# Optimization experiments

Hardware: AMD Instinct MI355X
Metric: run time of the kernel (lower is better)

## Reference

```python
import jax, jax.numpy as jnp
import numpy as np
from jax import lax

LBDA = 0.5   # soft-min temperature from OTAM_cum_dist_v2 default
EPS = 0.01   # cos_sim epsilon


def otam_cum_dist(dists, lbda=LBDA):
    """Soft-DTW-style OTAM DP. dists: [nq, ns, L, S] -> [nq, ns].
    Faithful to OTAM_cum_dist_v2: pad last dim by (1,1) with zeros, then run the
    row-wise recurrence. Soft-min computed via stable logsumexp (same math as
    -lbda*log(sum exp(-x/lbda)))."""
    nq, ns, L, S = dists.shape
    d = jnp.pad(dists, ((0, 0), (0, 0), (0, 0), (1, 1)))  # [nq, ns, L, W], W=S+2
    W = S + 2
    # Row 0: cum[0, m] = cum[0, m-1] + d[0, m], cum[0, 0] = 0
    row0 = jnp.concatenate(
        [jnp.zeros((nq, ns, 1), d.dtype), jnp.cumsum(d[:, :, 0, 1:], axis=-1)], axis=-1)
    if L == 1:
        return row0[..., -1]

    m_idx = jnp.arange(1, W)
    include_up = (m_idx == 1) | (m_idx == W - 1)  # only first/last cols use cum[l-1, m]
    INF = jnp.asarray(jnp.inf, d.dtype)

    def row_step(prev_row, d_row):
        # prev_row, d_row: [nq, ns, W]
        xs = (
            jnp.moveaxis(d_row[:, :, 1:], -1, 0),        # d[l, m],       [W-1, nq, ns]
            jnp.moveaxis(prev_row[:, :, :-1], -1, 0),    # cum[l-1, m-1]
            jnp.moveaxis(prev_row[:, :, 1:], -1, 0),     # cum[l-1, m]
            include_up,
        )

        def col_step(cur_left, x):
            d_m, p_diag, p_up, inc = x
            up = jnp.where(inc, p_up, INF)               # masked term -> exp(-inf)=0
            terms = jnp.stack([p_diag, cur_left, up])    # [3, nq, ns]
            new = d_m - lbda * jax.nn.logsumexp(-terms / lbda, axis=0)
            return new, new

        _, cols = lax.scan(col_step, jnp.zeros((nq, ns), d.dtype), xs)
        row = jnp.concatenate(
            [jnp.zeros((nq, ns, 1), d.dtype), jnp.moveaxis(cols, 0, -1)], axis=-1)
        return row, None

    d_rows = jnp.moveaxis(d[:, :, 1:, :], 2, 0)          # [L-1, nq, ns, W]
    final_row, _ = lax.scan(row_step, row0, d_rows)
    return final_row[..., -1]


def reference(support_features, query_features):
    """OTAM meta-logits (cum_dist_g = -otam_distance) of DSN_TEMPORAL.
    support_features: [n_classes, L, D] class prototypes; query_features: [nq, L, D]."""
    nq, Lq, D = query_features.shape
    ns, Ls, _ = support_features.shape
    q = query_features.reshape(nq * Lq, D)
    s = support_features.reshape(ns * Ls, D)
    # cos_sim with epsilon in denominator (faithful to cos_sim())
    num = q @ s.T
    den = (jnp.linalg.norm(q, axis=-1)[:, None]
           * jnp.linalg.norm(s, axis=-1)[None, :] + EPS)
    frame_dists = 1.0 - num / den                         # [nq*L, ns*S]
    dists = frame_dists.reshape(nq, Lq, ns, Ls).transpose(0, 2, 1, 3)  # [nq, ns, L, S]
    cum = otam_cum_dist(dists) + otam_cum_dist(dists.transpose(0, 1, 3, 2))
    return -cum                                           # meta_logits [nq, ns]


def setup_inputs() -> dict:
    key = jax.random.key(0)
    k1, k2 = jax.random.split(key)
    return {
        "support_features": jax.random.normal(k1, (64, 8, 576), dtype=jnp.float32),
        "query_features": jax.random.normal(k2, (2048, 8, 576), dtype=jnp.float32),
    }
```

## Files before the change

### kernel.cpp

```cpp
#include <hip/hip_runtime.h>

#define D_K 576
#define NSLAB 18
#define LBDA_INV 2.0f
#define HALF_LBDA 0.5f
#define EPS 0.01f
#define DSTRIDE 136
#define DT_STRIDE 72
#define POOL_USHORTS 17920

typedef __attribute__((ext_vector_type(8))) short short8;
typedef __attribute__((ext_vector_type(4))) float f32x4;

__device__ inline unsigned cvt_pk_bf16(float lo, float hi) {
    unsigned r;
    asm("v_cvt_pk_bf16_f32 %0, %1, %2" : "=v"(r) : "v"(lo), "v"(hi));
    return r;
}

__device__ inline float softmin2(float a, float b) {
    float mn = fminf(a, b), mx = fmaxf(a, b);
    return mn - HALF_LBDA * __logf(1.f + __expf(LBDA_INV * (mn - mx)));
}
__device__ inline float softmin3(float a, float b, float c) {
    float mn = fminf(fminf(a, b), c);
    float mx = fmaxf(fmaxf(a, b), c);
    float md = __builtin_amdgcn_fmed3f(a, b, c);
    float s = 1.f + __expf(LBDA_INV * (mn - md)) + __expf(LBDA_INV * (mn - mx));
    return mn - HALF_LBDA * __logf(s);
}

template <int STRIDE>
__device__ float otam_dp_rows(const unsigned short* base) {
    float x[8], prev[10], cur[10];
    auto load_row = [&](int l) {
        uint4 v = *(const uint4*)(base + l * STRIDE);
        x[0] = __uint_as_float(v.x << 16);
        x[1] = __uint_as_float(v.x & 0xFFFF0000u);
        x[2] = __uint_as_float(v.y << 16);
        x[3] = __uint_as_float(v.y & 0xFFFF0000u);
        x[4] = __uint_as_float(v.z << 16);
        x[5] = __uint_as_float(v.z & 0xFFFF0000u);
        x[6] = __uint_as_float(v.w << 16);
        x[7] = __uint_as_float(v.w & 0xFFFF0000u);
    };
    load_row(0);
    prev[0] = 0.f;
#pragma unroll
    for (int m = 1; m <= 8; ++m) prev[m] = prev[m - 1] + x[m - 1];
    prev[9] = prev[8];
#pragma unroll
    for (int l = 1; l < 8; ++l) {
        load_row(l);
        cur[0] = 0.f;
        cur[1] = x[0] + softmin3(prev[0], 0.f, prev[1]);
#pragma unroll
        for (int m = 2; m <= 8; ++m)
            cur[m] = x[m - 1] + softmin2(prev[m - 1], cur[m - 1]);
        cur[9] = softmin3(prev[8], cur[8], prev[9]);
#pragma unroll
        for (int m = 0; m < 10; ++m) prev[m] = cur[m];
    }
    return prev[9];
}

__global__ __launch_bounds__(256, 4) void fused_kernel(
        const float* __restrict__ sup, const float* __restrict__ qry,
        float* __restrict__ out) {
    __shared__ __align__(16) unsigned short pool[POOL_USHORTS];
    __shared__ float qn_l[64], sn_l[128];
    unsigned short* const As0 = pool;
    unsigned short* const Bs0 = pool + 2048;
    unsigned short* const As1 = pool + 6144;
    unsigned short* const Bs1 = pool + 8192;
    unsigned short* const Ds  = pool;
    unsigned short* const DsT = pool + 8704;

    const int t = threadIdx.x;
    const int b = blockIdx.x;
    const int xcd = b & 7, s2 = b >> 3;
    const int sblk = s2 >> 5;
    const int qh = xcd * 32 + (s2 & 31);

    const float* qsrc = qry + (size_t)qh * 64 * D_K;
    const float* ssrc = sup + (size_t)sblk * 128 * D_K;

    const int rr = t >> 3;
    const int cc = t & 7;
    const int c_in = cc >> 1, half = cc & 1;

    const int lane = t & 63;
    const int wave = t >> 6;
    const int wm = wave >> 1, wn = wave & 1;
    const int col16 = lane & 15, quad = lane >> 4;

    f32x4 acc[2][4];
#pragma unroll
    for (int i = 0; i < 2; ++i)
#pragma unroll
        for (int j = 0; j < 4; ++j) acc[i][j] = (f32x4){0.f, 0.f, 0.f, 0.f};

    int aoff[2], boff[4], woffA[2], woffB[4];
#pragma unroll
    for (int mt = 0; mt < 2; ++mt) {
        int m = wm * 32 + mt * 16 + col16;
        aoff[mt] = (quad * 64 + (m ^ (quad << 1))) * 8;
    }
#pragma unroll
    for (int nt = 0; nt < 4; ++nt) {
        int n = wn * 64 + nt * 16 + col16;
        boff[nt] = (quad * 128 + (n ^ (quad << 1))) * 8;
    }
#pragma unroll
    for (int j = 0; j < 2; ++j)
        woffA[j] = (c_in * 64 + ((j * 32 + rr) ^ (c_in << 1))) * 8 + half * 4;
#pragma unroll
    for (int j = 0; j < 4; ++j)
        woffB[j] = (c_in * 128 + ((j * 32 + rr) ^ (c_in << 1))) * 8 + half * 4;

    float ssA[2] = {0.f, 0.f}, ssB[4] = {0.f, 0.f, 0.f, 0.f};
    float4 va[2], vb[4];

    auto stage_load = [&](int sl) {
        const int off = sl * 32 + cc * 4;
#pragma unroll
        for (int j = 0; j < 2; ++j)
            va[j] = *(const float4*)(qsrc + (size_t)(j * 32 + rr) * D_K + off);
#pragma unroll
        for (int j = 0; j < 4; ++j)
            vb[j] = *(const float4*)(ssrc + (size_t)(j * 32 + rr) * D_K + off);
    };
    auto stage_write = [&](unsigned short* __restrict__ A,
                           unsigned short* __restrict__ B) {
#pragma unroll
        for (int j = 0; j < 2; ++j) {
            ssA[j] += va[j].x * va[j].x + va[j].y * va[j].y +
                      va[j].z * va[j].z + va[j].w * va[j].w;
            uint2 u;
            u.x = cvt_pk_bf16(va[j].x, va[j].y);
            u.y = cvt_pk_bf16(va[j].z, va[j].w);
            *(uint2*)(&A[woffA[j]]) = u;
        }
#pragma unroll
        for (int j = 0; j < 4; ++j) {
            ssB[j] += vb[j].x * vb[j].x + vb[j].y * vb[j].y +
                      vb[j].z * vb[j].z + vb[j].w * vb[j].w;
            uint2 u;
            u.x = cvt_pk_bf16(vb[j].x, vb[j].y);
            u.y = cvt_pk_bf16(vb[j].z, vb[j].w);
            *(uint2*)(&B[woffB[j]]) = u;
        }
    };
    auto compute = [&](const unsigned short* __restrict__ A,
                       const unsigned short* __restrict__ B) {
        short8 af[2], bq[4];
#pragma unroll
        for (int mt = 0; mt < 2; ++mt) af[mt] = *(const short8*)(&A[aoff[mt]]);
#pragma unroll
        for (int nt = 0; nt < 4; ++nt) bq[nt] = *(const short8*)(&B[boff[nt]]);
#pragma unroll
        for (int mt = 0; mt < 2; ++mt)
#pragma unroll
            for (int nt = 0; nt < 4; ++nt)
                acc[mt][nt] = __builtin_amdgcn_mfma_f32_16x16x32_bf16(
                    af[mt], bq[nt], acc[mt][nt], 0, 0, 0);
    };

    stage_load(0);
    stage_write(As0, Bs0);
    __syncthreads();

#pragma unroll 1
    for (int sp = 0; sp < 9; ++sp) {
        stage_load(2 * sp + 1);
        compute(As0, Bs0);
        stage_write(As1, Bs1);
        __syncthreads();
        if (sp < 8) stage_load(2 * sp + 2);
        compute(As1, Bs1);
        if (sp < 8) stage_write(As0, Bs0);
        __syncthreads();
    }

#pragma unroll
    for (int j = 0; j < 2; ++j) {
        float a = ssA[j];
        a += __shfl_down(a, 4); a += __shfl_down(a, 2); a += __shfl_down(a, 1);
        if ((t & 7) == 0) qn_l[j * 32 + rr] = sqrtf(a);
    }
#pragma unroll
    for (int j = 0; j < 4; ++j) {
        float s = ssB[j];
        s += __shfl_down(s, 4); s += __shfl_down(s, 2); s += __shfl_down(s, 1);
        if ((t & 7) == 0) sn_l[j * 32 + rr] = sqrtf(s);
    }
    __syncthreads();

#pragma unroll
    for (int mt = 0; mt < 2; ++mt) {
        const int m = wm * 32 + mt * 16 + quad * 4;
        float q0 = qn_l[m], q1 = qn_l[m + 1], q2 = qn_l[m + 2], q3 = qn_l[m + 3];
#pragma unroll
        for (int nt = 0; nt < 4; ++nt) {
            const int n = wn * 64 + nt * 16 + col16;
            float sv = sn_l[n];
            float d0 = 1.f - acc[mt][nt][0] * __builtin_amdgcn_rcpf(q0 * sv + EPS);
            float d1 = 1.f - acc[mt][nt][1] * __builtin_amdgcn_rcpf(q1 * sv + EPS);
            float d2 = 1.f - acc[mt][nt][2] * __builtin_amdgcn_rcpf(q2 * sv + EPS);
            float d3 = 1.f - acc[mt][nt][3] * __builtin_amdgcn_rcpf(q3 * sv + EPS);
            uint2 u;
            u.x = cvt_pk_bf16(d0, d1);
            u.y = cvt_pk_bf16(d2, d3);
            *(uint2*)(&DsT[n * DT_STRIDE + m]) = u;
            Ds[(m + 0) * DSTRIDE + n] = (unsigned short)(u.x);
            Ds[(m + 1) * DSTRIDE + n] = (unsigned short)(u.x >> 16);
            Ds[(m + 2) * DSTRIDE + n] = (unsigned short)(u.y);
            Ds[(m + 3) * DSTRIDE + n] = (unsigned short)(u.y >> 16);
        }
    }
    __syncthreads();

    const int p = t & 127, ql = p >> 4, sj = p & 15;
    float r;
    if (t < 128) {
        r = otam_dp_rows<DSTRIDE>(Ds + (ql * 8) * DSTRIDE + sj * 8);
    } else {
        r = otam_dp_rows<DT_STRIDE>(DsT + (sj * 8) * DT_STRIDE + ql * 8);
        sn_l[p] = r;
    }
    __syncthreads();
    if (t < 128) {
        int qg = qh * 8 + ql, sg = sblk * 16 + sj;
        out[qg * 64 + sg] = -(r + sn_l[p]);
    }
}

extern "C" void kernel_launch(void* const* d_in, const int* in_sizes, int n_in,
                              void* d_out, int out_size, void* d_ws, size_t ws_size,
                              hipStream_t stream) {
    const float* sup = (const float*)d_in[0];
    const float* qry = (const float*)d_in[1];
    float* out = (float*)d_out;
    (void)d_ws; (void)ws_size;
    fused_kernel<<<dim3(1024), dim3(256), 0, stream>>>(sup, qry, out);
}
```

Before: 105.6 us.

## Load query operand directly from global into MFMA registers, bypassing LDS

```diff
diff --git a/kernel.cpp b/kernel.cpp
--- a/kernel.cpp
+++ b/kernel.cpp
@@ -69,10 +69,8 @@
         float* __restrict__ out) {
     __shared__ __align__(16) unsigned short pool[POOL_USHORTS];
     __shared__ float qn_l[64], sn_l[128];
-    unsigned short* const As0 = pool;
-    unsigned short* const Bs0 = pool + 2048;
-    unsigned short* const As1 = pool + 6144;
-    unsigned short* const Bs1 = pool + 8192;
+    unsigned short* const Bs0 = pool;
+    unsigned short* const Bs1 = pool + 4096;
     unsigned short* const Ds  = pool;
     unsigned short* const DsT = pool + 8704;
 
@@ -100,47 +98,31 @@
 #pragma unroll
         for (int j = 0; j < 4; ++j) acc[i][j] = (f32x4){0.f, 0.f, 0.f, 0.f};
 
-    int aoff[2], boff[4], woffA[2], woffB[4];
-#pragma unroll
-    for (int mt = 0; mt < 2; ++mt) {
-        int m = wm * 32 + mt * 16 + col16;
-        aoff[mt] = (quad * 64 + (m ^ (quad << 1))) * 8;
-    }
+    int agoff[2];
+#pragma unroll
+    for (int mt = 0; mt < 2; ++mt)
+        agoff[mt] = (wm * 32 + mt * 16 + col16) * D_K + quad * 8;
+
+    int boff[4], woff[4];
 #pragma unroll
     for (int nt = 0; nt < 4; ++nt) {
         int n = wn * 64 + nt * 16 + col16;
         boff[nt] = (quad * 128 + (n ^ (quad << 1))) * 8;
     }
 #pragma unroll
-    for (int j = 0; j < 2; ++j)
-        woffA[j] = (c_in * 64 + ((j * 32 + rr) ^ (c_in << 1))) * 8 + half * 4;
-#pragma unroll
     for (int j = 0; j < 4; ++j)
-        woffB[j] = (c_in * 128 + ((j * 32 + rr) ^ (c_in << 1))) * 8 + half * 4;
+        woff[j] = (c_in * 128 + ((j * 32 + rr) ^ (c_in << 1))) * 8 + half * 4;
 
     float ssA[2] = {0.f, 0.f}, ssB[4] = {0.f, 0.f, 0.f, 0.f};
-    float4 va[2], vb[4];
+    float4 vb[4];
 
     auto stage_load = [&](int sl) {
         const int off = sl * 32 + cc * 4;
 #pragma unroll
-        for (int j = 0; j < 2; ++j)
-            va[j] = *(const float4*)(qsrc + (size_t)(j * 32 + rr) * D_K + off);
-#pragma unroll
         for (int j = 0; j < 4; ++j)
             vb[j] = *(const float4*)(ssrc + (size_t)(j * 32 + rr) * D_K + off);
     };
-    auto stage_write = [&](unsigned short* __restrict__ A,
-                           unsigned short* __restrict__ B) {
-#pragma unroll
-        for (int j = 0; j < 2; ++j) {
-            ssA[j] += va[j].x * va[j].x + va[j].y * va[j].y +
-                      va[j].z * va[j].z + va[j].w * va[j].w;
-            uint2 u;
-            u.x = cvt_pk_bf16(va[j].x, va[j].y);
-            u.y = cvt_pk_bf16(va[j].z, va[j].w);
-            *(uint2*)(&A[woffA[j]]) = u;
-        }
+    auto stage_write = [&](unsigned short* __restrict__ B) {
 #pragma unroll
         for (int j = 0; j < 4; ++j) {
             ssB[j] += vb[j].x * vb[j].x + vb[j].y * vb[j].y +
@@ -148,16 +130,34 @@
             uint2 u;
             u.x = cvt_pk_bf16(vb[j].x, vb[j].y);
             u.y = cvt_pk_bf16(vb[j].z, vb[j].w);
-            *(uint2*)(&B[woffB[j]]) = u;
-        }
-    };
-    auto compute = [&](const unsigned short* __restrict__ A,
-                       const unsigned short* __restrict__ B) {
-        short8 af[2], bq[4];
-#pragma unroll
-        for (int mt = 0; mt < 2; ++mt) af[mt] = *(const short8*)(&A[aoff[mt]]);
+            *(uint2*)(&B[woff[j]]) = u;
+        }
+    };
+    auto compute = [&](int sl, const unsigned short* __restrict__ B) {
+        float4 a0[2], a1[2];
+#pragma unroll
+        for (int mt = 0; mt < 2; ++mt) {
+            const float* ap = qsrc + agoff[mt] + sl * 32;
+            a0[mt] = *(const float4*)(ap);
+            a1[mt] = *(const float4*)(ap + 4);
+        }
+        short8 bq[4];
 #pragma unroll
         for (int nt = 0; nt < 4; ++nt) bq[nt] = *(const short8*)(&B[boff[nt]]);
+        short8 af[2];
+#pragma unroll
+        for (int mt = 0; mt < 2; ++mt) {
+            ssA[mt] += a0[mt].x * a0[mt].x + a0[mt].y * a0[mt].y +
+                       a0[mt].z * a0[mt].z + a0[mt].w * a0[mt].w +
+                       a1[mt].x * a1[mt].x + a1[mt].y * a1[mt].y +
+                       a1[mt].z * a1[mt].z + a1[mt].w * a1[mt].w;
+            uint4 u;
+            u.x = cvt_pk_bf16(a0[mt].x, a0[mt].y);
+            u.y = cvt_pk_bf16(a0[mt].z, a0[mt].w);
+            u.z = cvt_pk_bf16(a1[mt].x, a1[mt].y);
+            u.w = cvt_pk_bf16(a1[mt].z, a1[mt].w);
+            af[mt] = *(short8*)&u;
+        }
 #pragma unroll
         for (int mt = 0; mt < 2; ++mt)
 #pragma unroll
@@ -167,26 +167,27 @@
     };
 
     stage_load(0);
-    stage_write(As0, Bs0);
+    stage_write(Bs0);
     __syncthreads();
 
 #pragma unroll 1
     for (int sp = 0; sp < 9; ++sp) {
         stage_load(2 * sp + 1);
-        compute(As0, Bs0);
-        stage_write(As1, Bs1);
+        compute(2 * sp, Bs0);
+        stage_write(Bs1);
         __syncthreads();
         if (sp < 8) stage_load(2 * sp + 2);
-        compute(As1, Bs1);
-        if (sp < 8) stage_write(As0, Bs0);
+        compute(2 * sp + 1, Bs1);
+        if (sp < 8) stage_write(Bs0);
         __syncthreads();
     }
 
 #pragma unroll
-    for (int j = 0; j < 2; ++j) {
-        float a = ssA[j];
-        a += __shfl_down(a, 4); a += __shfl_down(a, 2); a += __shfl_down(a, 1);
-        if ((t & 7) == 0) qn_l[j * 32 + rr] = sqrtf(a);
+    for (int mt = 0; mt < 2; ++mt) {
+        float a = ssA[mt];
+        a += __shfl_down(a, 32);
+        a += __shfl_down(a, 16);
+        if (wn == 0 && lane < 16) qn_l[wm * 32 + mt * 16 + lane] = sqrtf(a);
     }
 #pragma unroll
     for (int j = 0; j < 4; ++j) {
```

New measurement: 127.1 us. +20.3%, slower.
